# Optimization experiments

Measured on AMD Instinct MI355X. Metric: run time of the kernel, lower is better.

The kernel has to match this reference:

```python
import jax, jax.numpy as jnp
import numpy as np

B, N, C, H = 32, 129, 768, 12
HID = 4 * C
EPS = 1e-5
NEG = -65504.0


def _layer_norm(x, g, b):
    mu = jnp.mean(x, axis=-1, keepdims=True)
    var = jnp.mean((x - mu) ** 2, axis=-1, keepdims=True)
    return (x - mu) / jnp.sqrt(var + EPS) * g + b


def _attn(x, m, g, b, wqkv, wproj):
    # x: [B, Nn, C], m: [B, Nn, 1] binary float mask
    Bb, Nn, Cc = x.shape
    hd = Cc // H
    xm = _layer_norm(x, g, b) * m
    qkv = (xm @ wqkv).reshape(Bb, Nn, 3, H, hd)
    q, k, v = (jnp.swapaxes(qkv[:, :, i], 1, 2) for i in range(3))  # [B,H,Nn,hd]
    att = jnp.einsum('bhqd,bhkd->bhqk', q, k) * (hd ** -0.5)
    outer = (m @ jnp.swapaxes(m, -1, -2))[:, None]  # [B,1,Nn,Nn] mask outer product
    att = jnp.where(outer == 0.0, NEG, att)
    att = jax.nn.softmax(att, axis=-1) * m[:, None]  # zero masked query rows
    out = jnp.einsum('bhqk,bhkd->bhqd', att, v)
    out = jnp.swapaxes(out, 1, 2).reshape(Bb, Nn, Cc)
    return out @ wproj


def _mlp(x, m, g, b, w1, w2):
    xm = _layer_norm(x, g, b) * m
    return jax.nn.gelu(xm @ w1, approximate=False) @ w2


def setup_inputs() -> dict:
    key = jax.random.key(0)
    ks = jax.random.split(key, 10)
    std = 0.02
    return {
        'RGB': jax.random.normal(ks[0], (B, N, C), jnp.float32),
        'NIR': jax.random.normal(ks[1], (B, N, C), jnp.float32),
        'TIR': jax.random.normal(ks[2], (B, N, C), jnp.float32),
        'mask': (jax.random.uniform(ks[3], (B, N - 1, 1)) > 0.3).astype(jnp.float32),
        'label': jax.random.randint(ks[4], (B,), 0, 171),
        # stacked params for branches [R, N, T, concat]
        'ln_g1': jnp.ones((4, C), jnp.float32),
        'ln_b1': jnp.zeros((4, C), jnp.float32),
        'w_qkv': std * jax.random.normal(ks[5], (4, C, 3 * C), jnp.float32),
        'w_proj': std * jax.random.normal(ks[6], (4, C, C), jnp.float32),
        'ln_g2': jnp.ones((4, C), jnp.float32),
        'ln_b2': jnp.zeros((4, C), jnp.float32),
        'w_fc1': std * jax.random.normal(ks[7], (4, C, HID), jnp.float32),
        'w_fc2': std * jax.random.normal(ks[8], (4, HID, C), jnp.float32),
        'out_g': jnp.ones((C,), jnp.float32),
        'out_b': jnp.zeros((C,), jnp.float32),
    }


def reference(RGB, NIR, TIR, mask, label, ln_g1, ln_b1, w_qkv, w_proj,
              ln_g2, ln_b2, w_fc1, w_fc2, out_g, out_b):
    m = jnp.concatenate([jnp.ones((RGB.shape[0], 1, 1), RGB.dtype), mask], axis=1)  # [B,N,1]

    def branch(x, i, mm):
        x = x + _attn(x, mm, ln_g1[i], ln_b1[i], w_qkv[i], w_proj[i])
        x = x + _mlp(x, mm, ln_g2[i], ln_b2[i], w_fc1[i], w_fc2[i])
        return x

    RGB = branch(RGB, 0, m)
    NIR = branch(NIR, 1, m)
    TIR = branch(TIR, 2, m)
    x = jnp.concatenate([RGB, NIR, TIR], axis=1)  # [B, 3N, C]
    m3 = jnp.tile(m, (1, 3, 1))
    x = branch(x, 3, m3)
    x = _layer_norm(x, out_g, out_b) * m3
    return x
```

## Files before the change

### kernel.cpp

```cpp
#include <hip/hip_runtime.h>

typedef unsigned short u16;
typedef __attribute__((ext_vector_type(4))) float f32x4;
typedef __attribute__((ext_vector_type(8))) short s16x8;
typedef __attribute__((ext_vector_type(4))) short s16x4;
typedef __attribute__((ext_vector_type(4))) unsigned short u16x4;

#define HH 12
#define CC 768
#define AS1(p) ((const __attribute__((address_space(1))) void*)(p))
#define AS3(p) ((__attribute__((address_space(3))) void*)(p))

__device__ inline u16 f2bf(float x){
  unsigned u = __float_as_uint(x);
  u = (u + 0x7FFFu + ((u >> 16) & 1u)) >> 16;
  return (u16)u;
}

__device__ inline f32x4 mfma32(s16x8 a, s16x8 b, f32x4 c){
  return __builtin_amdgcn_mfma_f32_16x16x32_bf16(a, b, c, 0, 0, 0);
}
__device__ inline f32x4 mfma16(s16x4 a, s16x4 b, f32x4 c){
  return __builtin_amdgcn_mfma_f32_16x16x16bf16_1k(a, b, c, 0, 0, 0);
}

__device__ inline void xcd_remap(int gx, int gy, int& bx, int& by){
  int nwg = gx*gy;
  int orig = blockIdx.x + gx*blockIdx.y;
  int q = nwg >> 3, r8 = nwg & 7;
  int xcd = orig & 7, off = orig >> 3;
  int wg = (xcd < r8 ? xcd*(q+1) : r8*(q+1) + (xcd-r8)*q) + off;
  bx = wg / gy; by = wg - bx*gy;
}

__device__ inline void epi_store(float v, int row, int col, void* O, size_t zsO,
                                 int z, int N, int zoffmul, int EPI, int TPB){
}

__global__ void wtrans(const float* __restrict__ W, u16* __restrict__ Wt, int K, int N){
  __shared__ float tile[32][33];
  int k0 = blockIdx.x*32, n0 = blockIdx.y*32;
  const float* Wz = W + (size_t)blockIdx.z*K*N;
  u16* Wtz = Wt + (size_t)blockIdx.z*K*N;
  int tx = threadIdx.x & 31, ty = threadIdx.x >> 5;
  #pragma unroll
  for(int r = ty; r < 32; r += 8)
    tile[r][tx] = Wz[(size_t)(k0+r)*N + n0 + tx];
  __syncthreads();
  #pragma unroll
  for(int r = ty; r < 32; r += 8)
    Wtz[(size_t)(n0+r)*K + k0 + tx] = f2bf(tile[tx][r]);
}

__global__ void initcat(const float* __restrict__ R, const float* __restrict__ Nr,
                        const float* __restrict__ T, float* __restrict__ xcat){
  int idx = blockIdx.x*256 + threadIdx.x;
  const int per = 32*129*768/4;
  if(idx >= per) return;
  int z = blockIdx.y;
  const float* src = z == 0 ? R : (z == 1 ? Nr : T);
  float4 v = ((const float4*)src)[idx];
  int e = idx*4;
  int row = e / 768, c = e - row*768;
  int bb2 = row / 129, nn = row - bb2*129;
  ((float4*)xcat)[((size_t)(bb2*387 + z*129 + nn)*768 + c)/4] = v;
}

__device__ inline float maskval(const float* m, int b, int n){
  return (n == 0) ? 1.0f : m[b*128 + n - 1];
}

template<int F32OUT>
__global__ __launch_bounds__(64) void ln_mask(
    const float* __restrict__ x,
    const float* __restrict__ gg, const float* __restrict__ bb, int zsG,
    const float* __restrict__ mask,
    void* __restrict__ out, size_t zsO,
    int tpb, int zoffmul)
{
  int r = blockIdx.x, z = blockIdx.y, lane = threadIdx.x;
  int bidx = r / tpb, nn = r - bidx*tpb;
  size_t cat = (size_t)bidx*387 + z*zoffmul + nn;
  const float4* xr = (const float4*)(x + cat*CC);
  float4 v[3]; float s = 0.f, sq = 0.f;
  #pragma unroll
  for(int w = 0; w < 3; ++w){
    v[w] = xr[w*64 + lane];
    s  += v[w].x + v[w].y + v[w].z + v[w].w;
    sq += v[w].x*v[w].x + v[w].y*v[w].y + v[w].z*v[w].z + v[w].w*v[w].w;
  }
  #pragma unroll
  for(int o = 32; o; o >>= 1){ s += __shfl_xor(s, o); sq += __shfl_xor(sq, o); }
  float mu = s * (1.f/768.f);
  float var = sq * (1.f/768.f) - mu*mu;
  float rstd = rsqrtf(var + 1e-5f);
  float mv = maskval(mask, bidx, nn % 129);
  const float4* g4 = (const float4*)(gg + (size_t)z*zsG);
  const float4* b4 = (const float4*)(bb + (size_t)z*zsG);
  #pragma unroll
  for(int w = 0; w < 3; ++w){
    float4 gv = g4[w*64+lane], bv = b4[w*64+lane];
    float y0 = ((v[w].x - mu)*rstd*gv.x + bv.x) * mv;
    float y1 = ((v[w].y - mu)*rstd*gv.y + bv.y) * mv;
    float y2 = ((v[w].z - mu)*rstd*gv.z + bv.z) * mv;
    float y3 = ((v[w].w - mu)*rstd*gv.w + bv.w) * mv;
    if(F32OUT){
      ((float4*)out)[cat*(CC/4) + w*64 + lane] = make_float4(y0,y1,y2,y3);
    } else {
      u16x4 p; p.x = f2bf(y0); p.y = f2bf(y1); p.z = f2bf(y2); p.w = f2bf(y3);
      ((u16x4*)((u16*)out + z*zsO + (size_t)r*CC))[w*64 + lane] = p;
    }
  }
}

template<int EPI, int TPB>
__global__ __launch_bounds__(256, 4) void gemm_bt(
    const u16* __restrict__ A, size_t zsA,
    const u16* __restrict__ Bt, size_t zsB,
    void* __restrict__ O, size_t zsO,
    int M, int N, int K,
    int zoffmul)
{
  __shared__ u16 As[128*64];
  __shared__ u16 Bs[128*64];
  int z = blockIdx.z;
  const u16* Az = A + zsA*(size_t)z;
  const u16* Bz = Bt + zsB*(size_t)z;
  int bx, by; xcd_remap(gridDim.x, gridDim.y, bx, by);
  int m0 = bx*128, n0 = by*128;

  int tid = threadIdx.x, wid = tid >> 6, lane = tid & 63;
  int wr = wid >> 1, wc = wid & 1;
  int lrow = lane & 15, g4 = lane >> 4;

  int srow = tid >> 3;
  int swcol = ((tid & 7) ^ (srow & 7)) * 8;
  const u16 *pa[4], *pb[4];
  #pragma unroll
  for(int i = 0; i < 4; ++i){
    int ra = m0 + srow + i*32; ra = ra < M ? ra : M - 1;
    pa[i] = Az + (size_t)ra*K + swcol;
    pb[i] = Bz + (size_t)(n0 + srow + i*32)*K + swcol;
  }
  int dofs = tid*8;
  int xs0 = ((0*4 + g4) ^ (lrow & 7)) * 8;
  int xs1 = ((1*4 + g4) ^ (lrow & 7)) * 8;

  f32x4 acc[4][4] = {};
  int NT = K >> 6;

  for(int t = 0; t < NT; ++t){
    #pragma unroll
    for(int i = 0; i < 4; ++i)
      __builtin_amdgcn_global_load_lds(AS1(pa[i]), AS3(&As[dofs + i*2048]), 16, 0, 0);
    #pragma unroll
    for(int i = 0; i < 4; ++i)
      __builtin_amdgcn_global_load_lds(AS1(pb[i]), AS3(&Bs[dofs + i*2048]), 16, 0, 0);
    #pragma unroll
    for(int i = 0; i < 4; ++i){ pa[i] += 64; pb[i] += 64; }
    __syncthreads();
    #pragma unroll
    for(int kk = 0; kk < 2; ++kk){
      int xs = kk ? xs1 : xs0;
      s16x8 aF[4], bF[4];
      #pragma unroll
      for(int i = 0; i < 4; ++i){
        aF[i] = *(const s16x8*)&As[(wr*64 + i*16 + lrow)*64 + xs];
        bF[i] = *(const s16x8*)&Bs[(wc*64 + i*16 + lrow)*64 + xs];
      }
      #pragma unroll
      for(int i = 0; i < 4; ++i)
        #pragma unroll
        for(int jn = 0; jn < 4; ++jn)
          acc[i][jn] = mfma32(aF[i], bF[jn], acc[i][jn]);
    }
    __syncthreads();
  }

  u16* Oz = (u16*)O + zsO*(size_t)z;
  int zb = z*zoffmul;
  #pragma unroll
  for(int i = 0; i < 4; ++i){
    #pragma unroll
    for(int r = 0; r < 4; ++r){
      int row = m0 + wr*64 + i*16 + g4*4 + r;
      if(row >= M) continue;
      #pragma unroll
      for(int jn = 0; jn < 4; ++jn){
        int col = n0 + wc*64 + jn*16 + lrow;
        float v = acc[i][jn][r];
        if constexpr (EPI == 0){
          Oz[(size_t)row*N + col] = f2bf(v);
        } else if constexpr (EPI == 1){
          float u = v*(0.7978845608f + 0.0356774081f*v*v);
          float t = 1.f - 2.f/(__expf(2.f*u) + 1.f);
          Oz[(size_t)row*N + col] = f2bf(0.5f*v*(1.f + t));
        } else {
          int bi = row / TPB, nnn = row - bi*TPB;
          size_t cat = (size_t)bi*387 + zb + nnn;
          float* dst = (float*)O + cat*CC + col;
          *dst += v;
        }
      }
    }
  }
}

template<int EPI, int TPB>
__global__ __launch_bounds__(512, 1) void gemm8(
    const u16* __restrict__ A, size_t zsA,
    const u16* __restrict__ Bt, size_t zsB,
    void* __restrict__ O, size_t zsO,
    int M, int N, int K,
    int zoffmul)
{
  __shared__ u16 As[2][256*64];
  __shared__ u16 Bs[2][256*64];
  int z = blockIdx.z;
  const u16* Az = A + zsA*(size_t)z;
  const u16* Bz = Bt + zsB*(size_t)z;
  int bx, by; xcd_remap(gridDim.x, gridDim.y, bx, by);
  int m0 = bx*256, n0 = by*256;

  int tid = threadIdx.x, wid = tid >> 6, lane = tid & 63;
  int wr = wid >> 2, wc = wid & 3;
  int lrow = lane & 15, g4 = lane >> 4;

  int srow = tid >> 3;
  int swcol = ((tid & 7) ^ (srow & 7)) * 8;
  const u16 *pa[4], *pb[4];
  #pragma unroll
  for(int i = 0; i < 4; ++i){
    int ra = m0 + srow + i*64; ra = ra < M ? ra : M - 1;
    pa[i] = Az + (size_t)ra*K + swcol;
    pb[i] = Bz + (size_t)(n0 + srow + i*64)*K + swcol;
  }
  int dofs = tid*8;

  int xsk[2];
  xsk[0] = ((0*4 + g4) ^ (lrow & 7)) * 8;
  xsk[1] = ((1*4 + g4) ^ (lrow & 7)) * 8;

  #pragma unroll
  for(int i = 0; i < 4; ++i)
    __builtin_amdgcn_global_load_lds(AS1(pa[i]), AS3(&As[0][dofs + i*4096]), 16, 0, 0);
  #pragma unroll
  for(int i = 0; i < 4; ++i)
    __builtin_amdgcn_global_load_lds(AS1(pb[i]), AS3(&Bs[0][dofs + i*4096]), 16, 0, 0);
  #pragma unroll
  for(int i = 0; i < 4; ++i){ pa[i] += 64; pb[i] += 64; }

  f32x4 acc[8][4] = {};
  int NT = K >> 6;

  for(int t = 0; t < NT; ++t){
    int cur = t & 1, nx = cur ^ 1;
    bool pf = (t + 1 < NT);
    s16x8 aF[4][2], bL[2][2], bH[2][2];

    if(pf){
      #pragma unroll
      for(int i = 0; i < 2; ++i)
        __builtin_amdgcn_global_load_lds(AS1(pa[i]), AS3(&As[nx][dofs + i*4096]), 16, 0, 0);
      asm volatile("s_waitcnt vmcnt(2)" ::: "memory");
    } else {
      asm volatile("s_waitcnt vmcnt(0)" ::: "memory");
    }
    asm volatile("s_barrier" ::: "memory");
    #pragma unroll
    for(int mi = 0; mi < 4; ++mi)
      #pragma unroll
      for(int ks = 0; ks < 2; ++ks)
        aF[mi][ks] = *(const s16x8*)&As[cur][(wr*128 + mi*16 + lrow)*64 + xsk[ks]];
    #pragma unroll
    for(int ni = 0; ni < 2; ++ni)
      #pragma unroll
      for(int ks = 0; ks < 2; ++ks)
        bL[ni][ks] = *(const s16x8*)&Bs[cur][(wc*64 + ni*16 + lrow)*64 + xsk[ks]];
    __builtin_amdgcn_s_setprio(1);
    #pragma unroll
    for(int mi = 0; mi < 4; ++mi)
      #pragma unroll
      for(int ni = 0; ni < 2; ++ni)
        #pragma unroll
        for(int ks = 0; ks < 2; ++ks)
          acc[mi][ni] = mfma32(aF[mi][ks], bL[ni][ks], acc[mi][ni]);
    __builtin_amdgcn_s_setprio(0);
    asm volatile("s_barrier" ::: "memory");

    #pragma unroll
    for(int ni = 0; ni < 2; ++ni)
      #pragma unroll
      for(int ks = 0; ks < 2; ++ks)
        bH[ni][ks] = *(const s16x8*)&Bs[cur][(wc*64 + (2+ni)*16 + lrow)*64 + xsk[ks]];
    if(pf){
      #pragma unroll
      for(int i = 2; i < 4; ++i)
        __builtin_amdgcn_global_load_lds(AS1(pa[i]), AS3(&As[nx][dofs + i*4096]), 16, 0, 0);
    }
    __builtin_amdgcn_s_setprio(1);
    #pragma unroll
    for(int mi = 0; mi < 4; ++mi)
      #pragma unroll
      for(int ni = 0; ni < 2; ++ni)
        #pragma unroll
        for(int ks = 0; ks < 2; ++ks)
          acc[mi][2+ni] = mfma32(aF[mi][ks], bH[ni][ks], acc[mi][2+ni]);
    __builtin_amdgcn_s_setprio(0);
    asm volatile("s_barrier" ::: "memory");

    #pragma unroll
    for(int mi = 0; mi < 4; ++mi)
      #pragma unroll
      for(int ks = 0; ks < 2; ++ks)
        aF[mi][ks] = *(const s16x8*)&As[cur][(wr*128 + (4+mi)*16 + lrow)*64 + xsk[ks]];
    if(pf){
      #pragma unroll
      for(int i = 0; i < 2; ++i)
        __builtin_amdgcn_global_load_lds(AS1(pb[i]), AS3(&Bs[nx][dofs + i*4096]), 16, 0, 0);
    }
    __builtin_amdgcn_s_setprio(1);
    #pragma unroll
    for(int mi = 0; mi < 4; ++mi)
      #pragma unroll
      for(int ni = 0; ni < 2; ++ni)
        #pragma unroll
        for(int ks = 0; ks < 2; ++ks)
          acc[4+mi][2+ni] = mfma32(aF[mi][ks], bH[ni][ks], acc[4+mi][2+ni]);
    __builtin_amdgcn_s_setprio(0);
    asm volatile("s_barrier" ::: "memory");

    if(pf){
      #pragma unroll
      for(int i = 2; i < 4; ++i)
        __builtin_amdgcn_global_load_lds(AS1(pb[i]), AS3(&Bs[nx][dofs + i*4096]), 16, 0, 0);
      #pragma unroll
      for(int i = 0; i < 4; ++i){ pa[i] += 64; pb[i] += 64; }
    }
    __builtin_amdgcn_s_setprio(1);
    #pragma unroll
    for(int mi = 0; mi < 4; ++mi)
      #pragma unroll
      for(int ni = 0; ni < 2; ++ni)
        #pragma unroll
        for(int ks = 0; ks < 2; ++ks)
          acc[4+mi][ni] = mfma32(aF[mi][ks], bL[ni][ks], acc[4+mi][ni]);
    __builtin_amdgcn_s_setprio(0);
    asm volatile("s_barrier" ::: "memory");
  }

  u16* Oz = (u16*)O + zsO*(size_t)z;
  int zb = z*zoffmul;
  #pragma unroll
  for(int mi = 0; mi < 8; ++mi){
    #pragma unroll
    for(int r = 0; r < 4; ++r){
      int row = m0 + wr*128 + mi*16 + g4*4 + r;
      if(row >= M) continue;
      #pragma unroll
      for(int ni = 0; ni < 4; ++ni){
        int col = n0 + wc*64 + ni*16 + lrow;
        float v = acc[mi][ni][r];
        if constexpr (EPI == 0){
          Oz[(size_t)row*N + col] = f2bf(v);
        } else if constexpr (EPI == 1){
          float u = v*(0.7978845608f + 0.0356774081f*v*v);
          float t = 1.f - 2.f/(__expf(2.f*u) + 1.f);
          Oz[(size_t)row*N + col] = f2bf(0.5f*v*(1.f + t));
        } else {
          int bi = row / TPB, nnn = row - bi*TPB;
          size_t cat = (size_t)bi*387 + zb + nnn;
          float* dst = (float*)O + cat*CC + col;
          *dst += v;
        }
      }
    }
  }
}

template<int N_>
__global__ __launch_bounds__(256) void attn3(
    const u16* __restrict__ qkv, size_t zsQ,
    u16* __restrict__ out, size_t zsO,
    const float* __restrict__ mask)
{
  constexpr int NC  = (N_ + 63)/64;
  constexpr int NKC = NC*64;
  constexpr float SCL = 0.125f*1.44269504088896f;
  __shared__ u16 Ks[2][64][66];
  __shared__ u16 Vt[2][64][68];
  __shared__ float Msk[NKC];

  int z = blockIdx.z;
  int bh = blockIdx.y, b = bh / HH, hh = bh - b*HH;
  int tid = threadIdx.x, wid = tid >> 6, lane = tid & 63;
  int lq = lane & 15, g = lane >> 4;
  const u16* qz = qkv + zsQ*(size_t)z;
  const size_t rowbase = (size_t)b*N_;
  const u16* kbase = qz + rowbase*2304 + 768 + hh*64;
  const u16* vbase = kbase + 768;

  for(int k = tid; k < NKC; k += 256){
    float mk = 0.f;
    if(k < N_){ int nn = (N_ > 129) ? (k % 129) : k; mk = (nn == 0) ? 1.f : mask[b*128 + nn - 1]; }
    Msk[k] = (mk != 0.f) ? 0.f : -1e30f;
  }

  int q0 = blockIdx.x*64 + wid*16;
  int qrow = q0 + lq;
  int qrc = qrow < N_ ? qrow : N_ - 1;
  const u16* qptr = qz + (rowbase + qrc)*2304 + hh*64;
  s16x8 qF0 = *(const s16x8*)(qptr + g*8);
  s16x8 qF1 = *(const s16x8*)(qptr + 32 + g*8);

  int r0 = tid >> 3, c16 = tid & 7;
  s16x8 kr[2], vr[2];
  const s16x8 zv = {0,0,0,0,0,0,0,0};

  #pragma unroll
  for(int i = 0; i < 2; ++i){
    int row = r0 + i*32;
    kr[i] = (row < N_) ? *(const s16x8*)(kbase + (size_t)row*2304 + c16*8) : zv;
    vr[i] = (row < N_) ? *(const s16x8*)(vbase + (size_t)row*2304 + c16*8) : zv;
  }
  #pragma unroll
  for(int i = 0; i < 2; ++i){
    *(s16x8*)&Ks[0][r0 + i*32][c16*8] = kr[i];
    #pragma unroll
    for(int j = 0; j < 8; ++j) Vt[0][c16*8 + j][r0 + i*32] = (u16)vr[i][j];
  }
  __syncthreads();

  f32x4 o[4] = {};
  float l = 0.f;

  for(int ch = 0; ch < NC; ++ch){
    int cur = ch & 1;
    if(ch + 1 < NC){
      #pragma unroll
      for(int i = 0; i < 2; ++i){
        int row = (ch + 1)*64 + r0 + i*32;
        kr[i] = (row < N_) ? *(const s16x8*)(kbase + (size_t)row*2304 + c16*8) : zv;
        vr[i] = (row < N_) ? *(const s16x8*)(vbase + (size_t)row*2304 + c16*8) : zv;
      }
    }
    float pT[4][4];
    #pragma unroll
    for(int t = 0; t < 4; ++t){
      s16x8 kF0 = *(const s16x8*)&Ks[cur][t*16 + lq][g*8];
      s16x8 kF1 = *(const s16x8*)&Ks[cur][t*16 + lq][32 + g*8];
      f32x4 s = {0.f,0.f,0.f,0.f};
      s = mfma32(kF0, qF0, s);
      s = mfma32(kF1, qF1, s);
      const float* mrow = &Msk[ch*64 + t*16 + g*4];
      #pragma unroll
      for(int r = 0; r < 4; ++r){
        float p = exp2f(fmaf(s[r], SCL, mrow[r]));
        pT[t][r] = p;
        l += p;
      }
    }
    #pragma unroll
    for(int t = 0; t < 4; ++t){
      s16x4 pa;
      #pragma unroll
      for(int r = 0; r < 4; ++r) pa[r] = (short)f2bf(pT[t][r]);
      #pragma unroll
      for(int db = 0; db < 4; ++db){
        s16x4 vf = *(const s16x4*)&Vt[cur][db*16 + lq][t*16 + g*4];
        o[db] = mfma16(pa, vf, o[db]);
      }
    }
    if(ch + 1 < NC){
      int nxt = (ch + 1) & 1;
      #pragma unroll
      for(int i = 0; i < 2; ++i){
        *(s16x8*)&Ks[nxt][r0 + i*32][c16*8] = kr[i];
        #pragma unroll
        for(int j = 0; j < 8; ++j) Vt[nxt][c16*8 + j][r0 + i*32] = (u16)vr[i][j];
      }
      __syncthreads();
    }
  }

  l += __shfl_xor(l, 16);
  l += __shfl_xor(l, 32);
  float mq = 0.f;
  if(qrow < N_) mq = (Msk[qrow] == 0.f) ? 1.f : 0.f;
  float sc = mq / l;
  float scr[4];
  #pragma unroll
  for(int r = 0; r < 4; ++r) scr[r] = __shfl(sc, g*4 + r);

  #pragma unroll
  for(int db = 0; db < 4; ++db){
    #pragma unroll
    for(int r = 0; r < 4; ++r){
      int qq = q0 + g*4 + r;
      if(qq < N_)
        out[zsO*(size_t)z + (rowbase + qq)*CC + hh*64 + db*16 + lq] = f2bf(o[db][r]*scr[r]);
    }
  }
}

extern "C" void kernel_launch(void* const* d_in, const int* in_sizes, int n_in,
                              void* d_out, int out_size, void* d_ws, size_t ws_size,
                              hipStream_t stream)
{
  const float* RGB   = (const float*)d_in[0];
  const float* NIR   = (const float*)d_in[1];
  const float* TIR   = (const float*)d_in[2];
  const float* mask  = (const float*)d_in[3];
  const float* ln_g1 = (const float*)d_in[5];
  const float* ln_b1 = (const float*)d_in[6];
  const float* w_qkv = (const float*)d_in[7];
  const float* w_proj= (const float*)d_in[8];
  const float* ln_g2 = (const float*)d_in[9];
  const float* ln_b2 = (const float*)d_in[10];
  const float* w_fc1 = (const float*)d_in[11];
  const float* w_fc2 = (const float*)d_in[12];
  const float* out_g = (const float*)d_in[13];
  const float* out_b = (const float*)d_in[14];

  char* p = (char*)d_ws;
  u16* wqkv_t  = (u16*)p; p += (size_t)4*2304*768*2;
  u16* wproj_t = (u16*)p; p += (size_t)4*768*768*2;
  u16* w1_t    = (u16*)p; p += (size_t)4*768*3072*2;
  u16* w2_t    = (u16*)p; p += (size_t)4*3072*768*2;
  float* xcat  = (float*)p; p += (size_t)12384*768*4;
  u16* xm      = (u16*)p; p += (size_t)3*4224*768*2;
  u16* qkv     = (u16*)p; p += (size_t)3*4224*3072*2;
  u16* hbuf    = qkv;
  if((size_t)(p - (char*)d_ws) > ws_size) return;

  wtrans<<<dim3(24, 72, 4), 256, 0, stream>>>(w_qkv, wqkv_t, 768, 2304);
  wtrans<<<dim3(24, 24, 4), 256, 0, stream>>>(w_proj, wproj_t, 768, 768);
  wtrans<<<dim3(24, 96, 4), 256, 0, stream>>>(w_fc1, w1_t, 768, 3072);
  wtrans<<<dim3(96, 24, 4), 256, 0, stream>>>(w_fc2, w2_t, 3072, 768);
  initcat<<<dim3(3096, 3), 256, 0, stream>>>(RGB, NIR, TIR, xcat);

  const int M3 = 4128;
  const size_t zxm = (size_t)4224*768, zqkv = (size_t)4224*2304, zh = (size_t)4224*3072;
  ln_mask<0><<<dim3(M3,3), 64, 0, stream>>>(xcat, ln_g1, ln_b1, 768, mask, xm, zxm, 129, 129);
  gemm8<0,1><<<dim3(17,9,3), 512, 0, stream>>>(xm, zxm, wqkv_t, (size_t)2304*768, qkv, zqkv, M3, 2304, 768, 0);
  attn3<129><<<dim3(3,384,3), 256, 0, stream>>>(qkv, zqkv, xm, zxm, mask);
  gemm_bt<2,129><<<dim3(33,6,3), 256, 0, stream>>>(xm, zxm, wproj_t, (size_t)768*768, xcat, 0, M3, 768, 768, 129);
  ln_mask<0><<<dim3(M3,3), 64, 0, stream>>>(xcat, ln_g2, ln_b2, 768, mask, xm, zxm, 129, 129);
  gemm8<1,1><<<dim3(17,12,3), 512, 0, stream>>>(xm, zxm, w1_t, (size_t)768*3072, hbuf, zh, M3, 3072, 768, 0);
  gemm8<2,129><<<dim3(17,3,3), 512, 0, stream>>>(hbuf, zh, w2_t, (size_t)768*3072, xcat, 0, M3, 768, 3072, 129);
  const int M1 = 12384;
  ln_mask<0><<<dim3(M1,1), 64, 0, stream>>>(xcat, ln_g1 + 3*768, ln_b1 + 3*768, 0, mask, xm, 0, 387, 0);
  gemm8<0,1><<<dim3(49,9,1), 512, 0, stream>>>(xm, 0, wqkv_t + (size_t)3*2304*768, 0, qkv, 0, M1, 2304, 768, 0);
  attn3<387><<<dim3(7,384,1), 256, 0, stream>>>(qkv, 0, xm, 0, mask);
  gemm_bt<2,387><<<dim3(97,6,1), 256, 0, stream>>>(xm, 0, wproj_t + (size_t)3*768*768, 0, xcat, 0, M1, 768, 768, 0);
  ln_mask<0><<<dim3(M1,1), 64, 0, stream>>>(xcat, ln_g2 + 3*768, ln_b2 + 3*768, 0, mask, xm, 0, 387, 0);
  gemm8<1,1><<<dim3(49,12,1), 512, 0, stream>>>(xm, 0, w1_t + (size_t)3*768*3072, 0, hbuf, 0, M1, 3072, 768, 0);
  gemm8<2,387><<<dim3(49,3,1), 512, 0, stream>>>(hbuf, 0, w2_t + (size_t)3*768*3072, 0, xcat, 0, M1, 768, 3072, 0);
  ln_mask<1><<<dim3(M1,1), 64, 0, stream>>>(xcat, out_g, out_b, 0, mask, d_out, 0, 387, 0);
}
```

Baseline: 818.6 us.

## Reschedule GEMM prefetch, batch LayerNorm rows per block, double attention queries per wave

The main GEMM loop moves its prefetch: all A-tile loads now issue after the first fragment reads and all B-tile loads after the second. A single vmcnt(0) wait before the last phase replaces the per-iteration partial waits, and sched_barrier fences stop the compiler from moving MFMAs across phases. LayerNorm now handles four rows per 256-thread block instead of one row per 64-thread block, which cuts block count and launch overhead. The attention kernel gives each wave two 16-query tiles so every K/V chunk loaded into LDS is reused twice, halving the grid, at the cost of more registers and less parallelism.

Result: no change. 826.7 us (+1.0%).

```diff
diff --git a/kernel.cpp b/kernel.cpp
--- a/kernel.cpp
+++ b/kernel.cpp
@@ -31,10 +31,6 @@
   int xcd = orig & 7, off = orig >> 3;
   int wg = (xcd < r8 ? xcd*(q+1) : r8*(q+1) + (xcd-r8)*q) + off;
   bx = wg / gy; by = wg - bx*gy;
-}
-
-__device__ inline void epi_store(float v, int row, int col, void* O, size_t zsO,
-                                 int z, int N, int zoffmul, int EPI, int TPB){
 }
 
 __global__ void wtrans(const float* __restrict__ W, u16* __restrict__ Wt, int K, int N){
@@ -71,14 +67,15 @@
 }
 
 template<int F32OUT>
-__global__ __launch_bounds__(64) void ln_mask(
+__global__ __launch_bounds__(256) void ln_mask(
     const float* __restrict__ x,
     const float* __restrict__ gg, const float* __restrict__ bb, int zsG,
     const float* __restrict__ mask,
     void* __restrict__ out, size_t zsO,
     int tpb, int zoffmul)
 {
-  int r = blockIdx.x, z = blockIdx.y, lane = threadIdx.x;
+  int wid = threadIdx.x >> 6, lane = threadIdx.x & 63;
+  int r = blockIdx.x*4 + wid, z = blockIdx.y;
   int bidx = r / tpb, nn = r - bidx*tpb;
   size_t cat = (size_t)bidx*387 + z*zoffmul + nn;
   const float4* xr = (const float4*)(x + cat*CC);
@@ -249,6 +246,8 @@
     __builtin_amdgcn_global_load_lds(AS1(pb[i]), AS3(&Bs[0][dofs + i*4096]), 16, 0, 0);
   #pragma unroll
   for(int i = 0; i < 4; ++i){ pa[i] += 64; pb[i] += 64; }
+  asm volatile("s_waitcnt vmcnt(0)" ::: "memory");
+  __builtin_amdgcn_s_barrier();
 
   f32x4 acc[8][4] = {};
   int NT = K >> 6;
@@ -258,15 +257,6 @@
     bool pf = (t + 1 < NT);
     s16x8 aF[4][2], bL[2][2], bH[2][2];
 
-    if(pf){
-      #pragma unroll
-      for(int i = 0; i < 2; ++i)
-        __builtin_amdgcn_global_load_lds(AS1(pa[i]), AS3(&As[nx][dofs + i*4096]), 16, 0, 0);
-      asm volatile("s_waitcnt vmcnt(2)" ::: "memory");
-    } else {
-      asm volatile("s_waitcnt vmcnt(0)" ::: "memory");
-    }
-    asm volatile("s_barrier" ::: "memory");
     #pragma unroll
     for(int mi = 0; mi < 4; ++mi)
       #pragma unroll
@@ -277,6 +267,13 @@
       #pragma unroll
       for(int ks = 0; ks < 2; ++ks)
         bL[ni][ks] = *(const s16x8*)&Bs[cur][(wc*64 + ni*16 + lrow)*64 + xsk[ks]];
+    if(pf){
+      #pragma unroll
+      for(int i = 0; i < 4; ++i)
+        __builtin_amdgcn_global_load_lds(AS1(pa[i]), AS3(&As[nx][dofs + i*4096]), 16, 0, 0);
+    }
+    __builtin_amdgcn_s_barrier();
+    __builtin_amdgcn_sched_barrier(0);
     __builtin_amdgcn_s_setprio(1);
     #pragma unroll
     for(int mi = 0; mi < 4; ++mi)
@@ -286,7 +283,7 @@
         for(int ks = 0; ks < 2; ++ks)
           acc[mi][ni] = mfma32(aF[mi][ks], bL[ni][ks], acc[mi][ni]);
     __builtin_amdgcn_s_setprio(0);
-    asm volatile("s_barrier" ::: "memory");
+    __builtin_amdgcn_s_barrier();
 
     #pragma unroll
     for(int ni = 0; ni < 2; ++ni)
@@ -295,9 +292,11 @@
         bH[ni][ks] = *(const s16x8*)&Bs[cur][(wc*64 + (2+ni)*16 + lrow)*64 + xsk[ks]];
     if(pf){
       #pragma unroll
-      for(int i = 2; i < 4; ++i)
-        __builtin_amdgcn_global_load_lds(AS1(pa[i]), AS3(&As[nx][dofs + i*4096]), 16, 0, 0);
-    }
+      for(int i = 0; i < 4; ++i)
+        __builtin_amdgcn_global_load_lds(AS1(pb[i]), AS3(&Bs[nx][dofs + i*4096]), 16, 0, 0);
+    }
+    __builtin_amdgcn_s_barrier();
+    __builtin_amdgcn_sched_barrier(0);
     __builtin_amdgcn_s_setprio(1);
     #pragma unroll
     for(int mi = 0; mi < 4; ++mi)
@@ -307,18 +306,15 @@
         for(int ks = 0; ks < 2; ++ks)
           acc[mi][2+ni] = mfma32(aF[mi][ks], bH[ni][ks], acc[mi][2+ni]);
     __builtin_amdgcn_s_setprio(0);
-    asm volatile("s_barrier" ::: "memory");
+    __builtin_amdgcn_s_barrier();
 
     #pragma unroll
     for(int mi = 0; mi < 4; ++mi)
       #pragma unroll
       for(int ks = 0; ks < 2; ++ks)
         aF[mi][ks] = *(const s16x8*)&As[cur][(wr*128 + (4+mi)*16 + lrow)*64 + xsk[ks]];
-    if(pf){
-      #pragma unroll
-      for(int i = 0; i < 2; ++i)
-        __builtin_amdgcn_global_load_lds(AS1(pb[i]), AS3(&Bs[nx][dofs + i*4096]), 16, 0, 0);
-    }
+    __builtin_amdgcn_s_barrier();
+    __builtin_amdgcn_sched_barrier(0);
     __builtin_amdgcn_s_setprio(1);
     #pragma unroll
     for(int mi = 0; mi < 4; ++mi)
@@ -328,15 +324,15 @@
         for(int ks = 0; ks < 2; ++ks)
           acc[4+mi][2+ni] = mfma32(aF[mi][ks], bH[ni][ks], acc[4+mi][2+ni]);
     __builtin_amdgcn_s_setprio(0);
-    asm volatile("s_barrier" ::: "memory");
+    __builtin_amdgcn_s_barrier();
 
     if(pf){
       #pragma unroll
-      for(int i = 2; i < 4; ++i)
-        __builtin_amdgcn_global_load_lds(AS1(pb[i]), AS3(&Bs[nx][dofs + i*4096]), 16, 0, 0);
-      #pragma unroll
       for(int i = 0; i < 4; ++i){ pa[i] += 64; pb[i] += 64; }
-    }
+      asm volatile("s_waitcnt vmcnt(0)" ::: "memory");
+    }
+    __builtin_amdgcn_s_barrier();
+    __builtin_amdgcn_sched_barrier(0);
     __builtin_amdgcn_s_setprio(1);
     #pragma unroll
     for(int mi = 0; mi < 4; ++mi)
@@ -346,7 +342,7 @@
         for(int ks = 0; ks < 2; ++ks)
           acc[4+mi][ni] = mfma32(aF[mi][ks], bL[ni][ks], acc[4+mi][ni]);
     __builtin_amdgcn_s_setprio(0);
-    asm volatile("s_barrier" ::: "memory");
+    __builtin_amdgcn_s_barrier();
   }
 
   u16* Oz = (u16*)O + zsO*(size_t)z;
@@ -406,12 +402,16 @@
     Msk[k] = (mk != 0.f) ? 0.f : -1e30f;
   }
 
-  int q0 = blockIdx.x*64 + wid*16;
-  int qrow = q0 + lq;
-  int qrc = qrow < N_ ? qrow : N_ - 1;
-  const u16* qptr = qz + (rowbase + qrc)*2304 + hh*64;
-  s16x8 qF0 = *(const s16x8*)(qptr + g*8);
-  s16x8 qF1 = *(const s16x8*)(qptr + 32 + g*8);
+  int q0[2]; s16x8 qF0[2], qF1[2];
+  #pragma unroll
+  for(int qi = 0; qi < 2; ++qi){
+    q0[qi] = blockIdx.x*128 + qi*64 + wid*16;
+    int qrow = q0[qi] + lq;
+    int qrc = qrow < N_ ? qrow : N_ - 1;
+    const u16* qptr = qz + (rowbase + qrc)*2304 + hh*64;
+    qF0[qi] = *(const s16x8*)(qptr + g*8);
+    qF1[qi] = *(const s16x8*)(qptr + 32 + g*8);
+  }
 
   int r0 = tid >> 3, c16 = tid & 7;
   s16x8 kr[2], vr[2];
@@ -431,8 +431,8 @@
   }
   __syncthreads();
 
-  f32x4 o[4] = {};
-  float l = 0.f;
+  f32x4 o[2][4] = {};
+  float l[2] = {0.f, 0.f};
 
   for(int ch = 0; ch < NC; ++ch){
     int cur = ch & 1;
@@ -444,31 +444,34 @@
         vr[i] = (row < N_) ? *(const s16x8*)(vbase + (size_t)row*2304 + c16*8) : zv;
       }
     }
-    float pT[4][4];
-    #pragma unroll
-    for(int t = 0; t < 4; ++t){
-      s16x8 kF0 = *(const s16x8*)&Ks[cur][t*16 + lq][g*8];
-      s16x8 kF1 = *(const s16x8*)&Ks[cur][t*16 + lq][32 + g*8];
-      f32x4 s = {0.f,0.f,0.f,0.f};
-      s = mfma32(kF0, qF0, s);
-      s = mfma32(kF1, qF1, s);
-      const float* mrow = &Msk[ch*64 + t*16 + g*4];
-      #pragma unroll
-      for(int r = 0; r < 4; ++r){
-        float p = exp2f(fmaf(s[r], SCL, mrow[r]));
-        pT[t][r] = p;
-        l += p;
-      }
-    }
-    #pragma unroll
-    for(int t = 0; t < 4; ++t){
-      s16x4 pa;
-      #pragma unroll
-      for(int r = 0; r < 4; ++r) pa[r] = (short)f2bf(pT[t][r]);
-      #pragma unroll
-      for(int db = 0; db < 4; ++db){
-        s16x4 vf = *(const s16x4*)&Vt[cur][db*16 + lq][t*16 + g*4];
-        o[db] = mfma16(pa, vf, o[db]);
+    #pragma unroll
+    for(int qi = 0; qi < 2; ++qi){
+      float pT[4][4];
+      #pragma unroll
+      for(int t = 0; t < 4; ++t){
+        s16x8 kF0 = *(const s16x8*)&Ks[cur][t*16 + lq][g*8];
+        s16x8 kF1 = *(const s16x8*)&Ks[cur][t*16 + lq][32 + g*8];
+        f32x4 s = {0.f,0.f,0.f,0.f};
+        s = mfma32(kF0, qF0[qi], s);
+        s = mfma32(kF1, qF1[qi], s);
+        const float* mrow = &Msk[ch*64 + t*16 + g*4];
+        #pragma unroll
+        for(int r = 0; r < 4; ++r){
+          float p = exp2f(fmaf(s[r], SCL, mrow[r]));
+          pT[t][r] = p;
+          l[qi] += p;
+        }
+      }
+      #pragma unroll
+      for(int t = 0; t < 4; ++t){
+        s16x4 pa;
+        #pragma unroll
+        for(int r = 0; r < 4; ++r) pa[r] = (short)f2bf(pT[t][r]);
+        #pragma unroll
+        for(int db = 0; db < 4; ++db){
+          s16x4 vf = *(const s16x4*)&Vt[cur][db*16 + lq][t*16 + g*4];
+          o[qi][db] = mfma16(pa, vf, o[qi][db]);
+        }
       }
     }
     if(ch + 1 < NC){
@@ -483,22 +486,26 @@
     }
   }
 
-  l += __shfl_xor(l, 16);
-  l += __shfl_xor(l, 32);
-  float mq = 0.f;
-  if(qrow < N_) mq = (Msk[qrow] == 0.f) ? 1.f : 0.f;
-  float sc = mq / l;
-  float scr[4];
-  #pragma unroll
-  for(int r = 0; r < 4; ++r) scr[r] = __shfl(sc, g*4 + r);
-
-  #pragma unroll
-  for(int db = 0; db < 4; ++db){
-    #pragma unroll
-    for(int r = 0; r < 4; ++r){
-      int qq = q0 + g*4 + r;
-      if(qq < N_)
-        out[zsO*(size_t)z + (rowbase + qq)*CC + hh*64 + db*16 + lq] = f2bf(o[db][r]*scr[r]);
+  #pragma unroll
+  for(int qi = 0; qi < 2; ++qi){
+    float lv = l[qi];
+    lv += __shfl_xor(lv, 16);
+    lv += __shfl_xor(lv, 32);
+    int qrow = q0[qi] + lq;
+    float mq = 0.f;
+    if(qrow < N_) mq = (Msk[qrow] == 0.f) ? 1.f : 0.f;
+    float sc = mq / lv;
+    float scr[4];
+    #pragma unroll
+    for(int r = 0; r < 4; ++r) scr[r] = __shfl(sc, g*4 + r);
+    #pragma unroll
+    for(int db = 0; db < 4; ++db){
+      #pragma unroll
+      for(int r = 0; r < 4; ++r){
+        int qq = q0[qi] + g*4 + r;
+        if(qq < N_)
+          out[zsO*(size_t)z + (rowbase + qq)*CC + hh*64 + db*16 + lq] = f2bf(o[qi][db][r]*scr[r]);
+      }
     }
   }
 }
@@ -541,20 +548,20 @@
 
   const int M3 = 4128;
   const size_t zxm = (size_t)4224*768, zqkv = (size_t)4224*2304, zh = (size_t)4224*3072;
-  ln_mask<0><<<dim3(M3,3), 64, 0, stream>>>(xcat, ln_g1, ln_b1, 768, mask, xm, zxm, 129, 129);
+  ln_mask<0><<<dim3(M3/4,3), 256, 0, stream>>>(xcat, ln_g1, ln_b1, 768, mask, xm, zxm, 129, 129);
   gemm8<0,1><<<dim3(17,9,3), 512, 0, stream>>>(xm, zxm, wqkv_t, (size_t)2304*768, qkv, zqkv, M3, 2304, 768, 0);
-  attn3<129><<<dim3(3,384,3), 256, 0, stream>>>(qkv, zqkv, xm, zxm, mask);
+  attn3<129><<<dim3(2,384,3), 256, 0, stream>>>(qkv, zqkv, xm, zxm, mask);
   gemm_bt<2,129><<<dim3(33,6,3), 256, 0, stream>>>(xm, zxm, wproj_t, (size_t)768*768, xcat, 0, M3, 768, 768, 129);
-  ln_mask<0><<<dim3(M3,3), 64, 0, stream>>>(xcat, ln_g2, ln_b2, 768, mask, xm, zxm, 129, 129);
+  ln_mask<0><<<dim3(M3/4,3), 256, 0, stream>>>(xcat, ln_g2, ln_b2, 768, mask, xm, zxm, 129, 129);
   gemm8<1,1><<<dim3(17,12,3), 512, 0, stream>>>(xm, zxm, w1_t, (size_t)768*3072, hbuf, zh, M3, 3072, 768, 0);
   gemm8<2,129><<<dim3(17,3,3), 512, 0, stream>>>(hbuf, zh, w2_t, (size_t)768*3072, xcat, 0, M3, 768, 3072, 129);
   const int M1 = 12384;
-  ln_mask<0><<<dim3(M1,1), 64, 0, stream>>>(xcat, ln_g1 + 3*768, ln_b1 + 3*768, 0, mask, xm, 0, 387, 0);
+  ln_mask<0><<<dim3(M1/4,1), 256, 0, stream>>>(xcat, ln_g1 + 3*768, ln_b1 + 3*768, 0, mask, xm, 0, 387, 0);
   gemm8<0,1><<<dim3(49,9,1), 512, 0, stream>>>(xm, 0, wqkv_t + (size_t)3*2304*768, 0, qkv, 0, M1, 2304, 768, 0);
-  attn3<387><<<dim3(7,384,1), 256, 0, stream>>>(qkv, 0, xm, 0, mask);
+  attn3<387><<<dim3(4,384,1), 256, 0, stream>>>(qkv, 0, xm, 0, mask);
   gemm_bt<2,387><<<dim3(97,6,1), 256, 0, stream>>>(xm, 0, wproj_t + (size_t)3*768*768, 0, xcat, 0, M1, 768, 768, 0);
-  ln_mask<0><<<dim3(M1,1), 64, 0, stream>>>(xcat, ln_g2 + 3*768, ln_b2 + 3*768, 0, mask, xm, 0, 387, 0);
+  ln_mask<0><<<dim3(M1/4,1), 256, 0, stream>>>(xcat, ln_g2 + 3*768, ln_b2 + 3*768, 0, mask, xm, 0, 387, 0);
   gemm8<1,1><<<dim3(49,12,1), 512, 0, stream>>>(xm, 0, w1_t + (size_t)3*768*3072, 0, hbuf, 0, M1, 3072, 768, 0);
   gemm8<2,387><<<dim3(49,3,1), 512, 0, stream>>>(hbuf, 0, w2_t + (size_t)3*768*3072, 0, xcat, 0, M1, 768, 3072, 0);
-  ln_mask<1><<<dim3(M1,1), 64, 0, stream>>>(xcat, out_g, out_b, 0, mask, d_out, 0, 387, 0);
-}
+  ln_mask<1><<<dim3(M1/4,1), 256, 0, stream>>>(xcat, out_g, out_b, 0, mask, d_out, 0, 387, 0);
+}
```
